# Kernel tuning notes

Measured on AMD Instinct MI355X. Metric: run time of the kernel, lower is better.

The kernel has to match this reference:

```python
import jax, jax.numpy as jnp
import numpy as np

N, D, H, C, OUT = 50000, 128, 2, 128, 2   # nodes, in-feat, heads, per-head width, classes
E = 800000
HC = H * C
NEG_SLOPE = 0.2


def setup_inputs() -> dict:
    key = jax.random.key(0)
    ks = jax.random.split(key, 12)
    x = jax.random.normal(ks[0], (N, D), dtype=jnp.float32)
    edge_index = jax.random.randint(ks[1], (2, E), 0, N, dtype=jnp.int64)
    def w(k, fan_in, shape):
        return jax.random.normal(k, shape, dtype=jnp.float32) / np.sqrt(fan_in)
    return {
        "x": x,
        "edge_index": edge_index,
        # layer 0: in D -> H*C
        "W0": w(ks[2], D, (D, HC)),
        "att_src0": w(ks[3], C, (H, C)),
        "att_dst0": w(ks[4], C, (H, C)),
        "b0": jnp.zeros((HC,), dtype=jnp.float32),
        # layer 1: in H*C -> H*C
        "W1": w(ks[5], HC, (HC, HC)),
        "att_src1": w(ks[6], C, (H, C)),
        "att_dst1": w(ks[7], C, (H, C)),
        "b1": jnp.zeros((HC,), dtype=jnp.float32),
        # final linear: H*C -> OUT (concat GAT output)
        "Wl": w(ks[8], HC, (HC, OUT)),
        "bl": jnp.zeros((OUT,), dtype=jnp.float32),
    }


def _gat_layer(x, src, dst, W, att_src, att_dst, b):
    """PyG GATConv (concat=True, negative_slope=0.2, self-loops already in src/dst)."""
    n = x.shape[0]
    h = (x @ W).reshape(n, H, C)                       # [N,H,C]
    a_s = jnp.einsum("nhc,hc->nh", h, att_src)         # [N,H]
    a_d = jnp.einsum("nhc,hc->nh", h, att_dst)         # [N,H]
    logits = jax.nn.leaky_relu(a_s[src] + a_d[dst], NEG_SLOPE)  # [E',H]
    m = jax.ops.segment_max(logits, dst, num_segments=n)
    e = jnp.exp(logits - m[dst])
    denom = jax.ops.segment_sum(e, dst, num_segments=n)
    alpha = e / (denom[dst] + 1e-16)                   # softmax over incoming edges
    msg = h[src] * alpha[:, :, None]                   # [E',H,C]
    out = jax.ops.segment_sum(msg, dst, num_segments=n)
    return out.reshape(n, HC) + b


def reference(x, edge_index, W0, att_src0, att_dst0, b0,
              W1, att_src1, att_dst1, b1, Wl, bl):
    n = x.shape[0]
    loop = jnp.arange(n, dtype=edge_index.dtype)
    src = jnp.concatenate([edge_index[0], loop])       # add self loops (GATConv default)
    dst = jnp.concatenate([edge_index[1], loop])
    h = _gat_layer(x, src, dst, W0, att_src0, att_dst0, b0)
    h = jnp.tanh(h)                                    # tanh between layers only
    h = _gat_layer(h, src, dst, W1, att_src1, att_dst1, b1)
    out = h @ Wl + bl
    return jax.nn.softmax(out, axis=1)
```

## Files before the change

kernel.cpp:

```cpp
#include <hip/hip_runtime.h>
#include <math.h>

constexpr int N_NODES = 50000;
constexpr int N_EDGES = 800000;
constexpr int TOT_E   = N_EDGES + N_NODES;
constexpr int HCv     = 256;
constexpr int MAXD    = 256;

constexpr int GY        = (N_NODES + 127) / 128;
constexpr int GPX       = (GY + 7) / 8;
constexpr int GEMM_BLKS = 8 * GPX * 4;

constexpr int PADSH = 5;

constexpr int PREP_CVT   = (N_NODES * 128 / 4 + 255) / 256;
constexpr int PREP_WT0   = 128;
constexpr int PREP_WT1   = 256;
constexpr int PREP_DEG   = (TOT_E + 255) / 256;
constexpr int PREP_ZERO  = (N_NODES * 12 / 4 + 255) / 256;
constexpr int PREP_C     = 1;
constexpr int PREP_BLKS  = PREP_CVT + PREP_WT0 + PREP_WT1 + PREP_DEG + PREP_ZERO + PREP_C;

typedef __attribute__((ext_vector_type(8))) short bf16x8;
typedef __attribute__((ext_vector_type(4))) float f32x4;
typedef __attribute__((ext_vector_type(2))) float f32x2;

__device__ __forceinline__ unsigned short f2bf(float f) {
    unsigned int u = __float_as_uint(f);
    unsigned int r = (u + 0x7fffu + ((u >> 16) & 1u)) >> 16;
    return (unsigned short)r;
}
__device__ __forceinline__ unsigned int f2bf_pack(float lo, float hi) {
    return (unsigned int)f2bf(lo) | ((unsigned int)f2bf(hi) << 16);
}
__device__ __forceinline__ float bf2f_lo(unsigned int packed) {
    return __uint_as_float(packed << 16);
}
__device__ __forceinline__ float bf2f_hi(unsigned int packed) {
    return __uint_as_float(packed & 0xffff0000u);
}

__device__ __forceinline__ void fma_row8_pk(const uint4 h, f32x2 al, f32x2* a2) {
    f32x2 p;
    p.x = bf2f_lo(h.x); p.y = bf2f_hi(h.x);
    a2[0] = __builtin_elementwise_fma(p, al, a2[0]);
    p.x = bf2f_lo(h.y); p.y = bf2f_hi(h.y);
    a2[1] = __builtin_elementwise_fma(p, al, a2[1]);
    p.x = bf2f_lo(h.z); p.y = bf2f_hi(h.z);
    a2[2] = __builtin_elementwise_fma(p, al, a2[2]);
    p.x = bf2f_lo(h.w); p.y = bf2f_hi(h.w);
    a2[3] = __builtin_elementwise_fma(p, al, a2[3]);
}


__global__ void zero_degp_k(uint4* __restrict__ degp4, int* __restrict__ total,
                            float* __restrict__ c2) {
    int i = blockIdx.x * blockDim.x + threadIdx.x;
    if (i < N_NODES * 32 / 4) degp4[i] = make_uint4(0, 0, 0, 0);
    if (blockIdx.x == 0 && threadIdx.x == 0) {
        *total = 0;
        c2[0] = 0.f;
        c2[1] = 0.f;
    }
}


__global__ __launch_bounds__(256) void prep_k(const float* __restrict__ x,
                                              unsigned short* __restrict__ xb,
                                              const float* __restrict__ W0,
                                              unsigned short* __restrict__ WT0,
                                              const float* __restrict__ W1,
                                              unsigned short* __restrict__ WT1,
                                              const int* __restrict__ ei,
                                              int* __restrict__ degp,
                                              float* __restrict__ a_sd,
                                              const float* __restrict__ Wl,
                                              const float* __restrict__ b1,
                                              const float* __restrict__ bl,
                                              float* __restrict__ c2) {
    int b = blockIdx.x;
    if (b < PREP_CVT) {
        int i = b * 256 + threadIdx.x;
        if (i < N_NODES * 128 / 4) {
            float4 v = *reinterpret_cast<const float4*>(x + (size_t)i * 4);
            ushort4 o;
            o.x = f2bf(v.x); o.y = f2bf(v.y); o.z = f2bf(v.z); o.w = f2bf(v.w);
            *reinterpret_cast<ushort4*>(xb + (size_t)i * 4) = o;
        }
        return;
    }
    b -= PREP_CVT;
    if (b < PREP_WT0) {
        int idx = b * 256 + threadIdx.x;
        int k = idx >> 8, n = idx & 255;
        WT0[(size_t)n * 128 + k] = f2bf(W0[idx]);
        return;
    }
    b -= PREP_WT0;
    if (b < PREP_WT1) {
        int idx = b * 256 + threadIdx.x;
        int k = idx >> 8, n = idx & 255;
        WT1[(size_t)n * 256 + k] = f2bf(W1[idx]);
        return;
    }
    b -= PREP_WT1;
    if (b < PREP_DEG) {
        int e = b * 256 + threadIdx.x;
        if (e < TOT_E) {
            int dst = (e < N_EDGES) ? ei[N_EDGES + e] : (e - N_EDGES);
            atomicAdd(&degp[dst << PADSH], 1);
        }
        return;
    }
    b -= PREP_DEG;
    if (b < PREP_ZERO) {
        int i = b * 256 + threadIdx.x;
        if (i < N_NODES * 3)
            *reinterpret_cast<float4*>(a_sd + (size_t)i * 4) = make_float4(0, 0, 0, 0);
        return;
    }
    {
        int k = threadIdx.x;
        int lane = k & 63;
        float bv = b1[k];
        float p0 = bv * Wl[k * 2 + 0];
        float p1 = bv * Wl[k * 2 + 1];
        if (k == 0) { p0 += bl[0]; p1 += bl[1]; }
#pragma unroll
        for (int off = 32; off; off >>= 1) {
            p0 += __shfl_xor(p0, off);
            p1 += __shfl_xor(p1, off);
        }
        if (lane == 0) {
            atomicAdd(&c2[0], p0);
            atomicAdd(&c2[1], p1);
        }
    }
}


__global__ void offsets_k(const int* __restrict__ degp, int* __restrict__ start,
                          int* __restrict__ deg, int* __restrict__ cursorp,
                          int* __restrict__ total) {
    int lane = threadIdx.x & 63;
    int node = blockIdx.x * blockDim.x + threadIdx.x;
    int d = (node < N_NODES) ? degp[node << PADSH] : 0;
    int pre = d;
#pragma unroll
    for (int off = 1; off < 64; off <<= 1) {
        int v = __shfl_up(pre, off);
        if (lane >= off) pre += v;
    }
    int wtot = __shfl(pre, 63);
    int base = 0;
    if (lane == 63) base = atomicAdd(total, wtot);
    base = __shfl(base, 63);
    int my = base + pre - d;
    if (node < N_NODES) {
        start[node] = my;
        deg[node] = d;
        cursorp[node << PADSH] = my;
    }
}

__global__ void scatter_k(const int* __restrict__ ei, int* __restrict__ cursorp,
                          int* __restrict__ colv) {
    int e = blockIdx.x * blockDim.x + threadIdx.x;
    if (e >= TOT_E) return;
    int srcv, dstv;
    if (e < N_EDGES) { srcv = ei[e]; dstv = ei[N_EDGES + e]; }
    else             { srcv = dstv = e - N_EDGES; }
    int pos = atomicAdd(&cursorp[dstv << PADSH], 1);
    colv[pos] = srcv;
}


template <int K, bool LAST>
__global__ __launch_bounds__(256) void mfma_gemm_att_k(
        const unsigned short* __restrict__ A,
        const unsigned short* __restrict__ BT,
        unsigned short* __restrict__ h16,
        const float* __restrict__ att_src, const float* __restrict__ att_dst,
        float* __restrict__ a_s, float* __restrict__ a_d, int M,
        const float* __restrict__ Wl, float* __restrict__ g) {
    const int bid = blockIdx.x;
    const int xcd = bid & 7;
    const int t   = bid >> 3;
    const int kx  = t & 3;
    const int gy  = xcd + 8 * (t >> 2);
    if (gy >= GY) return;

    const int lane = threadIdx.x & 63;
    const int wv = threadIdx.x >> 6;
    const int lm = lane & 15;
    const int g8 = (lane >> 4) * 8;
    const int row0 = gy * 128 + wv * 32;
    const int n0 = kx * 64;

    int ra0 = row0 + lm;       if (ra0 >= M) ra0 = M - 1;
    int ra1 = row0 + 16 + lm;  if (ra1 >= M) ra1 = M - 1;
    const unsigned short* pa0 = A + (size_t)ra0 * K + g8;
    const unsigned short* pa1 = A + (size_t)ra1 * K + g8;
    const unsigned short* pb  = BT + (size_t)(n0 + lm) * K + g8;

    f32x4 acc[2][4] = {};
#pragma unroll
    for (int kt = 0; kt < K; kt += 32) {
        bf16x8 a0 = *reinterpret_cast<const bf16x8*>(pa0 + kt);
        bf16x8 a1 = *reinterpret_cast<const bf16x8*>(pa1 + kt);
        bf16x8 b0 = *reinterpret_cast<const bf16x8*>(pb + kt);
        bf16x8 b1 = *reinterpret_cast<const bf16x8*>(pb + 16 * K + kt);
        bf16x8 b2 = *reinterpret_cast<const bf16x8*>(pb + 32 * K + kt);
        bf16x8 b3 = *reinterpret_cast<const bf16x8*>(pb + 48 * K + kt);
        acc[0][0] = __builtin_amdgcn_mfma_f32_16x16x32_bf16(a0, b0, acc[0][0], 0, 0, 0);
        acc[0][1] = __builtin_amdgcn_mfma_f32_16x16x32_bf16(a0, b1, acc[0][1], 0, 0, 0);
        acc[0][2] = __builtin_amdgcn_mfma_f32_16x16x32_bf16(a0, b2, acc[0][2], 0, 0, 0);
        acc[0][3] = __builtin_amdgcn_mfma_f32_16x16x32_bf16(a0, b3, acc[0][3], 0, 0, 0);
        acc[1][0] = __builtin_amdgcn_mfma_f32_16x16x32_bf16(a1, b0, acc[1][0], 0, 0, 0);
        acc[1][1] = __builtin_amdgcn_mfma_f32_16x16x32_bf16(a1, b1, acc[1][1], 0, 0, 0);
        acc[1][2] = __builtin_amdgcn_mfma_f32_16x16x32_bf16(a1, b2, acc[1][2], 0, 0, 0);
        acc[1][3] = __builtin_amdgcn_mfma_f32_16x16x32_bf16(a1, b3, acc[1][3], 0, 0, 0);
    }

    float as_c[4], ad_c[4], wl0_c[4], wl1_c[4];
#pragma unroll
    for (int j = 0; j < 4; ++j) {
        int c = n0 + j * 16 + lm;
        as_c[j] = att_src[c];
        ad_c[j] = att_dst[c];
        if (LAST) {
            wl0_c[j] = Wl[c * 2 + 0];
            wl1_c[j] = Wl[c * 2 + 1];
        }
    }
    const int head = n0 >> 7;

#pragma unroll
    for (int i = 0; i < 2; ++i) {
        float ps[4] = {}, pd[4] = {}, pg0[4] = {}, pg1[4] = {};
#pragma unroll
        for (int j = 0; j < 4; ++j)
#pragma unroll
            for (int r = 0; r < 4; ++r) {
                ps[r] += acc[i][j][r] * as_c[j];
                pd[r] += acc[i][j][r] * ad_c[j];
                if (LAST) {
                    pg0[r] += acc[i][j][r] * wl0_c[j];
                    pg1[r] += acc[i][j][r] * wl1_c[j];
                }
            }
#pragma unroll
        for (int off = 1; off < 16; off <<= 1)
#pragma unroll
            for (int r = 0; r < 4; ++r) {
                ps[r] += __shfl_xor(ps[r], off);
                pd[r] += __shfl_xor(pd[r], off);
                if (LAST) {
                    pg0[r] += __shfl_xor(pg0[r], off);
                    pg1[r] += __shfl_xor(pg1[r], off);
                }
            }
        if (lm == 0) {
            int rb = row0 + i * 16 + (lane >> 4) * 4;
#pragma unroll
            for (int r = 0; r < 4; ++r) {
                if (rb + r < M) {
                    atomicAdd(&a_s[(rb + r) * 2 + head], ps[r]);
                    atomicAdd(&a_d[(rb + r) * 2 + head], pd[r]);
                    if (LAST) {
                        atomicAdd(&g[(rb + r) * 4 + head * 2 + 0], pg0[r]);
                        atomicAdd(&g[(rb + r) * 4 + head * 2 + 1], pg1[r]);
                    }
                }
            }
        }
        if (!LAST) {
#pragma unroll
            for (int j = 0; j < 4; ++j)
#pragma unroll
                for (int r = 0; r < 4; ++r) {
                    int row = row0 + i * 16 + (lane >> 4) * 4 + r;
                    if (row < M)
                        h16[(size_t)row * HCv + n0 + j * 16 + lm] = f2bf(acc[i][j][r]);
                }
        }
    }
}


__device__ __forceinline__ float lrelu(float x) { return x > 0.f ? x : 0.2f * x; }

__global__ __launch_bounds__(256) void agg_k(const unsigned short* __restrict__ h16,
                      const float* __restrict__ a_s, const float* __restrict__ a_d,
                      const int* __restrict__ start, const int* __restrict__ deg,
                      const int* __restrict__ colv, const float* __restrict__ bias,
                      unsigned short* __restrict__ out16) {
    __shared__ float lexp[4][MAXD][2];
    const int lane = threadIdx.x & 63;
    const int wslot = threadIdx.x >> 6;
    const int node = blockIdx.x * 4 + wslot;
    if (node >= N_NODES) return;
    const int beg = start[node];
    const int degv = deg[node];
    const float ad0 = a_d[node * 2], ad1 = a_d[node * 2 + 1];
    const int* __restrict__ col = colv + beg;

    if (degv <= MAXD) {
        float s0 = 0.f, s1 = 0.f;
        for (int j = lane; j < degv; j += 64) {
            int s = col[j];
            float2 av = *reinterpret_cast<const float2*>(a_s + s * 2);
            float e0 = __expf(lrelu(av.x + ad0));
            float e1 = __expf(lrelu(av.y + ad1));
            *reinterpret_cast<float2*>(&lexp[wslot][j][0]) = make_float2(e0, e1);
            s0 += e0;
            s1 += e1;
        }
#pragma unroll
        for (int off = 32; off; off >>= 1) {
            s0 += __shfl_xor(s0, off);
            s1 += __shfl_xor(s1, off);
        }
        const float inv0 = 1.f / (s0 + 1e-16f);
        const float inv1 = 1.f / (s1 + 1e-16f);

        const int q = lane >> 4;
        const int lq = lane & 15;
        const int cb = lq * 16;
        const int head = lq >> 3;
        const float invh = head ? inv1 : inv0;
        const unsigned short* __restrict__ hp = h16 + cb;
        f32x2 acc2[8] = {};
        const int full = degv >> 2;
        for (int i = 0; i < full; ++i) {
            const int j = 4 * i + q;
            const int s = col[j];
            const float alpha = lexp[wslot][j][head] * invh;
            const f32x2 al = {alpha, alpha};
            const uint4* p = reinterpret_cast<const uint4*>(hp + (size_t)s * HCv);
            const uint4 h0 = p[0];
            const uint4 h1 = p[1];
            fma_row8_pk(h0, al, acc2);
            fma_row8_pk(h1, al, acc2 + 4);
        }
        {
            const int j = full * 4 + q;
            if (j < degv) {
                const int s = col[j];
                const float alpha = lexp[wslot][j][head] * invh;
                const f32x2 al = {alpha, alpha};
                const uint4* p = reinterpret_cast<const uint4*>(hp + (size_t)s * HCv);
                const uint4 h0 = p[0];
                const uint4 h1 = p[1];
                fma_row8_pk(h0, al, acc2);
                fma_row8_pk(h1, al, acc2 + 4);
            }
        }
        float acc[16];
#pragma unroll
        for (int c = 0; c < 8; ++c) {
            acc[2 * c]     = acc2[c].x;
            acc[2 * c + 1] = acc2[c].y;
        }
#pragma unroll
        for (int c = 0; c < 16; ++c) {
            acc[c] += __shfl_xor(acc[c], 16);
            acc[c] += __shfl_xor(acc[c], 32);
        }
        if (lane < 16) {
#pragma unroll
            for (int c = 0; c < 16; ++c) acc[c] = tanhf(acc[c] + bias[cb + c]);
            uint4 v0, v1;
            v0.x = f2bf_pack(acc[0], acc[1]);
            v0.y = f2bf_pack(acc[2], acc[3]);
            v0.z = f2bf_pack(acc[4], acc[5]);
            v0.w = f2bf_pack(acc[6], acc[7]);
            v1.x = f2bf_pack(acc[8], acc[9]);
            v1.y = f2bf_pack(acc[10], acc[11]);
            v1.z = f2bf_pack(acc[12], acc[13]);
            v1.w = f2bf_pack(acc[14], acc[15]);
            uint4* o = reinterpret_cast<uint4*>(out16 + (size_t)node * HCv + cb);
            o[0] = v0;
            o[1] = v1;
        }
    } else {
        const int end = beg + degv;
        float m0 = -INFINITY, m1 = -INFINITY;
        for (int e = beg + lane; e < end; e += 64) {
            int s = colv[e];
            m0 = fmaxf(m0, lrelu(a_s[s * 2] + ad0));
            m1 = fmaxf(m1, lrelu(a_s[s * 2 + 1] + ad1));
        }
#pragma unroll
        for (int off = 32; off; off >>= 1) {
            m0 = fmaxf(m0, __shfl_xor(m0, off));
            m1 = fmaxf(m1, __shfl_xor(m1, off));
        }
        float s0 = 0.f, s1 = 0.f;
        for (int e = beg + lane; e < end; e += 64) {
            int s = colv[e];
            s0 += __expf(lrelu(a_s[s * 2] + ad0) - m0);
            s1 += __expf(lrelu(a_s[s * 2 + 1] + ad1) - m1);
        }
#pragma unroll
        for (int off = 32; off; off >>= 1) {
            s0 += __shfl_xor(s0, off);
            s1 += __shfl_xor(s1, off);
        }
        float inv0 = 1.f / (s0 + 1e-16f);
        float inv1 = 1.f / (s1 + 1e-16f);
        const int head = lane >> 5;
        const float mh  = head ? m1 : m0;
        const float ih  = head ? inv1 : inv0;
        const float adh = head ? ad1 : ad0;
        const int cbase = lane * 4;
        float acc0 = 0.f, acc1 = 0.f, acc2 = 0.f, acc3 = 0.f;
        for (int e = beg; e < end; ++e) {
            int s = colv[e];
            float l = lrelu(a_s[s * 2 + head] + adh);
            float alpha = __expf(l - mh) * ih;
            uint2 hv = *reinterpret_cast<const uint2*>(h16 + (size_t)s * HCv + cbase);
            acc0 = fmaf(bf2f_lo(hv.x), alpha, acc0);
            acc1 = fmaf(bf2f_hi(hv.x), alpha, acc1);
            acc2 = fmaf(bf2f_lo(hv.y), alpha, acc2);
            acc3 = fmaf(bf2f_hi(hv.y), alpha, acc3);
        }
        float o0 = tanhf(acc0 + bias[cbase + 0]);
        float o1 = tanhf(acc1 + bias[cbase + 1]);
        float o2 = tanhf(acc2 + bias[cbase + 2]);
        float o3 = tanhf(acc3 + bias[cbase + 3]);
        ushort4 v;
        v.x = f2bf(o0); v.y = f2bf(o1); v.z = f2bf(o2); v.w = f2bf(o3);
        *reinterpret_cast<ushort4*>(out16 + (size_t)node * HCv + cbase) = v;
    }
}


__global__ __launch_bounds__(256) void agg_final_k(
        const float* __restrict__ a_s, const float* __restrict__ a_d,
        const float* __restrict__ g, const int* __restrict__ start,
        const int* __restrict__ deg, const int* __restrict__ colv,
        const float* __restrict__ c2, float* __restrict__ out) {
    const int lane = threadIdx.x & 63;
    const int node = blockIdx.x * 4 + (threadIdx.x >> 6);
    if (node >= N_NODES) return;
    const int beg = start[node];
    const int degv = deg[node];
    const float ad0 = a_d[node * 2], ad1 = a_d[node * 2 + 1];
    const int* __restrict__ col = colv + beg;

    float s0 = 0.f, s1 = 0.f, A00 = 0.f, A01 = 0.f, A10 = 0.f, A11 = 0.f;
    for (int j = lane; j < degv; j += 64) {
        int s = col[j];
        float2 av = *reinterpret_cast<const float2*>(a_s + s * 2);
        float4 gv = *reinterpret_cast<const float4*>(g + s * 4);
        float e0 = __expf(lrelu(av.x + ad0));
        float e1 = __expf(lrelu(av.y + ad1));
        s0 += e0;
        s1 += e1;
        A00 = fmaf(e0, gv.x, A00);
        A01 = fmaf(e0, gv.y, A01);
        A10 = fmaf(e1, gv.z, A10);
        A11 = fmaf(e1, gv.w, A11);
    }
#pragma unroll
    for (int off = 32; off; off >>= 1) {
        s0  += __shfl_xor(s0, off);
        s1  += __shfl_xor(s1, off);
        A00 += __shfl_xor(A00, off);
        A01 += __shfl_xor(A01, off);
        A10 += __shfl_xor(A10, off);
        A11 += __shfl_xor(A11, off);
    }
    if (lane == 0) {
        float i0 = 1.f / (s0 + 1e-16f), i1 = 1.f / (s1 + 1e-16f);
        float z0 = A00 * i0 + A10 * i1 + c2[0];
        float z1 = A01 * i0 + A11 * i1 + c2[1];
        float mx = fmaxf(z0, z1);
        float e0 = __expf(z0 - mx), e1 = __expf(z1 - mx);
        float inv = 1.f / (e0 + e1);
        out[node * 2 + 0] = e0 * inv;
        out[node * 2 + 1] = e1 * inv;
    }
}


extern "C" void kernel_launch(void* const* d_in, const int* in_sizes, int n_in,
                              void* d_out, int out_size, void* d_ws, size_t ws_size,
                              hipStream_t stream) {
    const float* x        = (const float*)d_in[0];
    const int*   ei       = (const int*)d_in[1];
    const float* W0       = (const float*)d_in[2];
    const float* att_src0 = (const float*)d_in[3];
    const float* att_dst0 = (const float*)d_in[4];
    const float* b0       = (const float*)d_in[5];
    const float* W1       = (const float*)d_in[6];
    const float* att_src1 = (const float*)d_in[7];
    const float* att_dst1 = (const float*)d_in[8];
    const float* b1       = (const float*)d_in[9];
    const float* Wl       = (const float*)d_in[10];
    const float* bl       = (const float*)d_in[11];
    float* out = (float*)d_out;

    unsigned short* xb     = (unsigned short*)d_ws;
    unsigned short* h16    = xb + (size_t)N_NODES * 128;
    unsigned short* hact16 = h16 + (size_t)N_NODES * HCv;
    unsigned short* WT0    = hact16 + (size_t)N_NODES * HCv;
    unsigned short* WT1    = WT0 + 256 * 128;
    int*   degp  = (int*)(WT1 + 256 * 256);
    float* a_sd  = (float*)(degp + (size_t)N_NODES * 32);
    float* as0   = a_sd;
    float* ad0   = as0 + N_NODES * 2;
    float* as1   = ad0 + N_NODES * 2;
    float* ad1   = as1 + N_NODES * 2;
    float* gbuf  = ad1 + N_NODES * 2;
    int* cursorp = (int*)(gbuf + (size_t)N_NODES * 4);
    int* deg     = cursorp + (size_t)N_NODES * 32;
    int* start   = deg + N_NODES;
    int* total   = start + N_NODES;
    float* c2    = (float*)(total + 1);
    int* colv    = (int*)(c2 + 2);

    zero_degp_k<<<(N_NODES * 32 / 4 + 255) / 256, 256, 0, stream>>>((uint4*)degp,
                                                                    total, c2);
    prep_k<<<PREP_BLKS, 256, 0, stream>>>(x, xb, W0, WT0, W1, WT1, ei, degp, a_sd,
                                          Wl, b1, bl, c2);

    offsets_k<<<(N_NODES + 255) / 256, 256, 0, stream>>>(degp, start, deg, cursorp, total);
    scatter_k<<<(TOT_E + 255) / 256, 256, 0, stream>>>(ei, cursorp, colv);

    int nn4 = (N_NODES + 3) / 4;

    mfma_gemm_att_k<128, false><<<GEMM_BLKS, 256, 0, stream>>>(
        xb, WT0, h16, att_src0, att_dst0, as0, ad0, N_NODES, nullptr, nullptr);
    agg_k<<<nn4, 256, 0, stream>>>(h16, as0, ad0, start, deg, colv, b0, hact16);

    mfma_gemm_att_k<256, true><<<GEMM_BLKS, 256, 0, stream>>>(
        hact16, WT1, nullptr, att_src1, att_dst1, as1, ad1, N_NODES, Wl, gbuf);
    agg_final_k<<<nn4, 256, 0, stream>>>(as1, ad1, gbuf, start, deg, colv, c2, out);
}
```

Before: 315.9 us.

## Aggregate raw features before the layer-0 GEMM and fold W1 into per-node projections

```diff
diff --git a/kernel.cpp b/kernel.cpp
--- a/kernel.cpp
+++ b/kernel.cpp
@@ -13,13 +13,13 @@
 
 constexpr int PADSH = 5;
 
-constexpr int PREP_CVT   = (N_NODES * 128 / 4 + 255) / 256;
-constexpr int PREP_WT0   = 128;
-constexpr int PREP_WT1   = 256;
-constexpr int PREP_DEG   = (TOT_E + 255) / 256;
-constexpr int PREP_ZERO  = (N_NODES * 12 / 4 + 255) / 256;
-constexpr int PREP_C     = 1;
-constexpr int PREP_BLKS  = PREP_CVT + PREP_WT0 + PREP_WT1 + PREP_DEG + PREP_ZERO + PREP_C;
+constexpr int PREP_CVT  = (N_NODES * 128 / 4 + 255) / 256;
+constexpr int PREP_WT0  = 128;
+constexpr int PREP_DEG  = (TOT_E + 255) / 256;
+constexpr int PREP_ZA   = (N_NODES * 8 / 4 + 255) / 256;
+constexpr int PREP_SKIN = (N_NODES + 15) / 16;
+constexpr int PREP_C    = 1;
+constexpr int PREP_BLKS = PREP_CVT + PREP_WT0 + PREP_DEG + PREP_ZA + PREP_SKIN + PREP_C;
 
 typedef __attribute__((ext_vector_type(8))) short bf16x8;
 typedef __attribute__((ext_vector_type(4))) float f32x4;
@@ -40,44 +40,68 @@
     return __uint_as_float(packed & 0xffff0000u);
 }
 
-__device__ __forceinline__ void fma_row8_pk(const uint4 h, f32x2 al, f32x2* a2) {
-    f32x2 p;
-    p.x = bf2f_lo(h.x); p.y = bf2f_hi(h.x);
-    a2[0] = __builtin_elementwise_fma(p, al, a2[0]);
-    p.x = bf2f_lo(h.y); p.y = bf2f_hi(h.y);
-    a2[1] = __builtin_elementwise_fma(p, al, a2[1]);
-    p.x = bf2f_lo(h.z); p.y = bf2f_hi(h.z);
-    a2[2] = __builtin_elementwise_fma(p, al, a2[2]);
-    p.x = bf2f_lo(h.w); p.y = bf2f_hi(h.w);
-    a2[3] = __builtin_elementwise_fma(p, al, a2[3]);
-}
-
-
-__global__ void zero_degp_k(uint4* __restrict__ degp4, int* __restrict__ total,
-                            float* __restrict__ c2) {
+__device__ __forceinline__ float lrelu(float x) { return x > 0.f ? x : 0.2f * x; }
+
+
+__global__ __launch_bounds__(256) void zero_pre_k(uint4* __restrict__ degp4,
+        int* __restrict__ total, float* __restrict__ c2,
+        const float* __restrict__ W0, const float* __restrict__ att_src0,
+        const float* __restrict__ att_dst0,
+        const float* __restrict__ W1, const float* __restrict__ att_src1,
+        const float* __restrict__ att_dst1, const float* __restrict__ Wl,
+        float* __restrict__ w0buf, float* __restrict__ pv) {
     int i = blockIdx.x * blockDim.x + threadIdx.x;
     if (i < N_NODES * 32 / 4) degp4[i] = make_uint4(0, 0, 0, 0);
-    if (blockIdx.x == 0 && threadIdx.x == 0) {
-        *total = 0;
-        c2[0] = 0.f;
-        c2[1] = 0.f;
+    if (blockIdx.x == 0) {
+        if (threadIdx.x == 0) { *total = 0; c2[0] = 0.f; c2[1] = 0.f; }
+        int k = threadIdx.x;
+        float v0 = 0, v1 = 0, v2 = 0, v3 = 0, v4 = 0, v5 = 0, v6 = 0, v7 = 0;
+        const float* wr = W1 + (size_t)k * 256;
+        for (int c = 0; c < 128; ++c) {
+            float wv = wr[c];
+            v0 = fmaf(wv, att_src1[c], v0);
+            v2 = fmaf(wv, att_dst1[c], v2);
+            v4 = fmaf(wv, Wl[c * 2 + 0], v4);
+            v5 = fmaf(wv, Wl[c * 2 + 1], v5);
+        }
+        for (int c = 128; c < 256; ++c) {
+            float wv = wr[c];
+            v1 = fmaf(wv, att_src1[c], v1);
+            v3 = fmaf(wv, att_dst1[c], v3);
+            v6 = fmaf(wv, Wl[c * 2 + 0], v6);
+            v7 = fmaf(wv, Wl[c * 2 + 1], v7);
+        }
+        float* p = pv + (size_t)k * 8;
+        p[0] = v0; p[1] = v1; p[2] = v2; p[3] = v3;
+        p[4] = v4; p[5] = v5; p[6] = v6; p[7] = v7;
+        if (k < 128) {
+            float w0v = 0, w1v = 0, w2v = 0, w3v = 0;
+            const float* wr0 = W0 + (size_t)k * 256;
+            for (int c = 0; c < 128; ++c) {
+                float wv = wr0[c];
+                w0v = fmaf(wv, att_src0[c], w0v);
+                w2v = fmaf(wv, att_dst0[c], w2v);
+            }
+            for (int c = 128; c < 256; ++c) {
+                float wv = wr0[c];
+                w1v = fmaf(wv, att_src0[c], w1v);
+                w3v = fmaf(wv, att_dst0[c], w3v);
+            }
+            float* q = w0buf + (size_t)k * 4;
+            q[0] = w0v; q[1] = w1v; q[2] = w2v; q[3] = w3v;
+        }
     }
 }
 
 
 __global__ __launch_bounds__(256) void prep_k(const float* __restrict__ x,
-                                              unsigned short* __restrict__ xb,
-                                              const float* __restrict__ W0,
-                                              unsigned short* __restrict__ WT0,
-                                              const float* __restrict__ W1,
-                                              unsigned short* __restrict__ WT1,
-                                              const int* __restrict__ ei,
-                                              int* __restrict__ degp,
-                                              float* __restrict__ a_sd,
-                                              const float* __restrict__ Wl,
-                                              const float* __restrict__ b1,
-                                              const float* __restrict__ bl,
-                                              float* __restrict__ c2) {
+        unsigned short* __restrict__ xb, const float* __restrict__ W0,
+        unsigned short* __restrict__ WT0, const int* __restrict__ ei,
+        int* __restrict__ degp, float* __restrict__ asd1,
+        const float* __restrict__ w0buf, float* __restrict__ a_s,
+        float* __restrict__ a_d, const float* __restrict__ Wl,
+        const float* __restrict__ b1, const float* __restrict__ bl,
+        float* __restrict__ c2) {
     int b = blockIdx.x;
     if (b < PREP_CVT) {
         int i = b * 256 + threadIdx.x;
@@ -97,13 +121,6 @@
         return;
     }
     b -= PREP_WT0;
-    if (b < PREP_WT1) {
-        int idx = b * 256 + threadIdx.x;
-        int k = idx >> 8, n = idx & 255;
-        WT1[(size_t)n * 256 + k] = f2bf(W1[idx]);
-        return;
-    }
-    b -= PREP_WT1;
     if (b < PREP_DEG) {
         int e = b * 256 + threadIdx.x;
         if (e < TOT_E) {
@@ -113,10 +130,43 @@
         return;
     }
     b -= PREP_DEG;
-    if (b < PREP_ZERO) {
+    if (b < PREP_ZA) {
         int i = b * 256 + threadIdx.x;
-        if (i < N_NODES * 3)
-            *reinterpret_cast<float4*>(a_sd + (size_t)i * 4) = make_float4(0, 0, 0, 0);
+        if (i < N_NODES * 2)
+            *reinterpret_cast<float4*>(asd1 + (size_t)i * 4) = make_float4(0, 0, 0, 0);
+        return;
+    }
+    b -= PREP_ZA;
+    if (b < PREP_SKIN) {
+        int lane = threadIdx.x & 63;
+        int sub = lane >> 4;
+        int lq = lane & 15;
+        int node = b * 16 + (threadIdx.x >> 6) * 4 + sub;
+        if (node < N_NODES) {
+            const float* xr = x + (size_t)node * 128 + lq * 8;
+            const float4* wv = reinterpret_cast<const float4*>(w0buf) + lq * 8;
+            float s0 = 0, s1 = 0, d0 = 0, d1 = 0;
+#pragma unroll
+            for (int t = 0; t < 8; ++t) {
+                float xv = xr[t];
+                float4 w = wv[t];
+                s0 = fmaf(xv, w.x, s0);
+                s1 = fmaf(xv, w.y, s1);
+                d0 = fmaf(xv, w.z, d0);
+                d1 = fmaf(xv, w.w, d1);
+            }
+#pragma unroll
+            for (int off = 1; off < 16; off <<= 1) {
+                s0 += __shfl_xor(s0, off);
+                s1 += __shfl_xor(s1, off);
+                d0 += __shfl_xor(d0, off);
+                d1 += __shfl_xor(d1, off);
+            }
+            if (lq == 0) {
+                *reinterpret_cast<float2*>(a_s + node * 2) = make_float2(s0, s1);
+                *reinterpret_cast<float2*>(a_d + node * 2) = make_float2(d0, d1);
+            }
+        }
         return;
     }
     {
@@ -175,126 +225,11 @@
 }
 
 
-template <int K, bool LAST>
-__global__ __launch_bounds__(256) void mfma_gemm_att_k(
-        const unsigned short* __restrict__ A,
-        const unsigned short* __restrict__ BT,
-        unsigned short* __restrict__ h16,
-        const float* __restrict__ att_src, const float* __restrict__ att_dst,
-        float* __restrict__ a_s, float* __restrict__ a_d, int M,
-        const float* __restrict__ Wl, float* __restrict__ g) {
-    const int bid = blockIdx.x;
-    const int xcd = bid & 7;
-    const int t   = bid >> 3;
-    const int kx  = t & 3;
-    const int gy  = xcd + 8 * (t >> 2);
-    if (gy >= GY) return;
-
-    const int lane = threadIdx.x & 63;
-    const int wv = threadIdx.x >> 6;
-    const int lm = lane & 15;
-    const int g8 = (lane >> 4) * 8;
-    const int row0 = gy * 128 + wv * 32;
-    const int n0 = kx * 64;
-
-    int ra0 = row0 + lm;       if (ra0 >= M) ra0 = M - 1;
-    int ra1 = row0 + 16 + lm;  if (ra1 >= M) ra1 = M - 1;
-    const unsigned short* pa0 = A + (size_t)ra0 * K + g8;
-    const unsigned short* pa1 = A + (size_t)ra1 * K + g8;
-    const unsigned short* pb  = BT + (size_t)(n0 + lm) * K + g8;
-
-    f32x4 acc[2][4] = {};
-#pragma unroll
-    for (int kt = 0; kt < K; kt += 32) {
-        bf16x8 a0 = *reinterpret_cast<const bf16x8*>(pa0 + kt);
-        bf16x8 a1 = *reinterpret_cast<const bf16x8*>(pa1 + kt);
-        bf16x8 b0 = *reinterpret_cast<const bf16x8*>(pb + kt);
-        bf16x8 b1 = *reinterpret_cast<const bf16x8*>(pb + 16 * K + kt);
-        bf16x8 b2 = *reinterpret_cast<const bf16x8*>(pb + 32 * K + kt);
-        bf16x8 b3 = *reinterpret_cast<const bf16x8*>(pb + 48 * K + kt);
-        acc[0][0] = __builtin_amdgcn_mfma_f32_16x16x32_bf16(a0, b0, acc[0][0], 0, 0, 0);
-        acc[0][1] = __builtin_amdgcn_mfma_f32_16x16x32_bf16(a0, b1, acc[0][1], 0, 0, 0);
-        acc[0][2] = __builtin_amdgcn_mfma_f32_16x16x32_bf16(a0, b2, acc[0][2], 0, 0, 0);
-        acc[0][3] = __builtin_amdgcn_mfma_f32_16x16x32_bf16(a0, b3, acc[0][3], 0, 0, 0);
-        acc[1][0] = __builtin_amdgcn_mfma_f32_16x16x32_bf16(a1, b0, acc[1][0], 0, 0, 0);
-        acc[1][1] = __builtin_amdgcn_mfma_f32_16x16x32_bf16(a1, b1, acc[1][1], 0, 0, 0);
-        acc[1][2] = __builtin_amdgcn_mfma_f32_16x16x32_bf16(a1, b2, acc[1][2], 0, 0, 0);
-        acc[1][3] = __builtin_amdgcn_mfma_f32_16x16x32_bf16(a1, b3, acc[1][3], 0, 0, 0);
-    }
-
-    float as_c[4], ad_c[4], wl0_c[4], wl1_c[4];
-#pragma unroll
-    for (int j = 0; j < 4; ++j) {
-        int c = n0 + j * 16 + lm;
-        as_c[j] = att_src[c];
-        ad_c[j] = att_dst[c];
-        if (LAST) {
-            wl0_c[j] = Wl[c * 2 + 0];
-            wl1_c[j] = Wl[c * 2 + 1];
-        }
-    }
-    const int head = n0 >> 7;
-
-#pragma unroll
-    for (int i = 0; i < 2; ++i) {
-        float ps[4] = {}, pd[4] = {}, pg0[4] = {}, pg1[4] = {};
-#pragma unroll
-        for (int j = 0; j < 4; ++j)
-#pragma unroll
-            for (int r = 0; r < 4; ++r) {
-                ps[r] += acc[i][j][r] * as_c[j];
-                pd[r] += acc[i][j][r] * ad_c[j];
-                if (LAST) {
-                    pg0[r] += acc[i][j][r] * wl0_c[j];
-                    pg1[r] += acc[i][j][r] * wl1_c[j];
-                }
-            }
-#pragma unroll
-        for (int off = 1; off < 16; off <<= 1)
-#pragma unroll
-            for (int r = 0; r < 4; ++r) {
-                ps[r] += __shfl_xor(ps[r], off);
-                pd[r] += __shfl_xor(pd[r], off);
-                if (LAST) {
-                    pg0[r] += __shfl_xor(pg0[r], off);
-                    pg1[r] += __shfl_xor(pg1[r], off);
-                }
-            }
-        if (lm == 0) {
-            int rb = row0 + i * 16 + (lane >> 4) * 4;
-#pragma unroll
-            for (int r = 0; r < 4; ++r) {
-                if (rb + r < M) {
-                    atomicAdd(&a_s[(rb + r) * 2 + head], ps[r]);
-                    atomicAdd(&a_d[(rb + r) * 2 + head], pd[r]);
-                    if (LAST) {
-                        atomicAdd(&g[(rb + r) * 4 + head * 2 + 0], pg0[r]);
-                        atomicAdd(&g[(rb + r) * 4 + head * 2 + 1], pg1[r]);
-                    }
-                }
-            }
-        }
-        if (!LAST) {
-#pragma unroll
-            for (int j = 0; j < 4; ++j)
-#pragma unroll
-                for (int r = 0; r < 4; ++r) {
-                    int row = row0 + i * 16 + (lane >> 4) * 4 + r;
-                    if (row < M)
-                        h16[(size_t)row * HCv + n0 + j * 16 + lm] = f2bf(acc[i][j][r]);
-                }
-        }
-    }
-}
-
-
-__device__ __forceinline__ float lrelu(float x) { return x > 0.f ? x : 0.2f * x; }
-
-__global__ __launch_bounds__(256) void agg_k(const unsigned short* __restrict__ h16,
+__global__ __launch_bounds__(256) void agg0x_k(const unsigned short* __restrict__ xb,
                       const float* __restrict__ a_s, const float* __restrict__ a_d,
                       const int* __restrict__ start, const int* __restrict__ deg,
-                      const int* __restrict__ colv, const float* __restrict__ bias,
-                      unsigned short* __restrict__ out16) {
+                      const int* __restrict__ colv,
+                      unsigned short* __restrict__ xagg) {
     __shared__ float lexp[4][MAXD][2];
     const int lane = threadIdx.x & 63;
     const int wslot = threadIdx.x >> 6;
@@ -326,41 +261,61 @@
 
         const int q = lane >> 4;
         const int lq = lane & 15;
-        const int cb = lq * 16;
-        const int head = lq >> 3;
-        const float invh = head ? inv1 : inv0;
-        const unsigned short* __restrict__ hp = h16 + cb;
-        f32x2 acc2[8] = {};
+        const unsigned short* __restrict__ xp = xb + lq * 8;
+        f32x2 aA[4] = {};
+        f32x2 aB[4] = {};
         const int full = degv >> 2;
         for (int i = 0; i < full; ++i) {
             const int j = 4 * i + q;
             const int s = col[j];
-            const float alpha = lexp[wslot][j][head] * invh;
-            const f32x2 al = {alpha, alpha};
-            const uint4* p = reinterpret_cast<const uint4*>(hp + (size_t)s * HCv);
-            const uint4 h0 = p[0];
-            const uint4 h1 = p[1];
-            fma_row8_pk(h0, al, acc2);
-            fma_row8_pk(h1, al, acc2 + 4);
+            float2 ee = *reinterpret_cast<float2*>(&lexp[wslot][j][0]);
+            const uint4 hv = *reinterpret_cast<const uint4*>(xp + (size_t)s * 128);
+            const f32x2 al0 = {ee.x, ee.x};
+            const f32x2 al1 = {ee.y, ee.y};
+            f32x2 p;
+            p.x = bf2f_lo(hv.x); p.y = bf2f_hi(hv.x);
+            aA[0] = __builtin_elementwise_fma(p, al0, aA[0]);
+            aB[0] = __builtin_elementwise_fma(p, al1, aB[0]);
+            p.x = bf2f_lo(hv.y); p.y = bf2f_hi(hv.y);
+            aA[1] = __builtin_elementwise_fma(p, al0, aA[1]);
+            aB[1] = __builtin_elementwise_fma(p, al1, aB[1]);
+            p.x = bf2f_lo(hv.z); p.y = bf2f_hi(hv.z);
+            aA[2] = __builtin_elementwise_fma(p, al0, aA[2]);
+            aB[2] = __builtin_elementwise_fma(p, al1, aB[2]);
+            p.x = bf2f_lo(hv.w); p.y = bf2f_hi(hv.w);
+            aA[3] = __builtin_elementwise_fma(p, al0, aA[3]);
+            aB[3] = __builtin_elementwise_fma(p, al1, aB[3]);
         }
         {
             const int j = full * 4 + q;
             if (j < degv) {
                 const int s = col[j];
-                const float alpha = lexp[wslot][j][head] * invh;
-                const f32x2 al = {alpha, alpha};
-                const uint4* p = reinterpret_cast<const uint4*>(hp + (size_t)s * HCv);
-                const uint4 h0 = p[0];
-                const uint4 h1 = p[1];
-                fma_row8_pk(h0, al, acc2);
-                fma_row8_pk(h1, al, acc2 + 4);
+                float2 ee = *reinterpret_cast<float2*>(&lexp[wslot][j][0]);
+                const uint4 hv = *reinterpret_cast<const uint4*>(xp + (size_t)s * 128);
+                const f32x2 al0 = {ee.x, ee.x};
+                const f32x2 al1 = {ee.y, ee.y};
+                f32x2 p;
+                p.x = bf2f_lo(hv.x); p.y = bf2f_hi(hv.x);
+                aA[0] = __builtin_elementwise_fma(p, al0, aA[0]);
+                aB[0] = __builtin_elementwise_fma(p, al1, aB[0]);
+                p.x = bf2f_lo(hv.y); p.y = bf2f_hi(hv.y);
+                aA[1] = __builtin_elementwise_fma(p, al0, aA[1]);
+                aB[1] = __builtin_elementwise_fma(p, al1, aB[1]);
+                p.x = bf2f_lo(hv.z); p.y = bf2f_hi(hv.z);
+                aA[2] = __builtin_elementwise_fma(p, al0, aA[2]);
+                aB[2] = __builtin_elementwise_fma(p, al1, aB[2]);
+                p.x = bf2f_lo(hv.w); p.y = bf2f_hi(hv.w);
+                aA[3] = __builtin_elementwise_fma(p, al0, aA[3]);
+                aB[3] = __builtin_elementwise_fma(p, al1, aB[3]);
             }
         }
         float acc[16];
 #pragma unroll
-        for (int c = 0; c < 8; ++c) {
-            acc[2 * c]     = acc2[c].x;
-            acc[2 * c + 1] = acc2[c].y;
+        for (int c = 0; c < 4; ++c) {
+            acc[2 * c]     = aA[c].x;
+            acc[2 * c + 1] = aA[c].y;
+            acc[8 + 2 * c]     = aB[c].x;
+            acc[8 + 2 * c + 1] = aB[c].y;
         }
 #pragma unroll
         for (int c = 0; c < 16; ++c) {
@@ -369,7 +324,9 @@
         }
         if (lane < 16) {
 #pragma unroll
-            for (int c = 0; c < 16; ++c) acc[c] = tanhf(acc[c] + bias[cb + c]);
+            for (int c = 0; c < 8; ++c)  acc[c] *= inv0;
+#pragma unroll
+            for (int c = 8; c < 16; ++c) acc[c] *= inv1;
             uint4 v0, v1;
             v0.x = f2bf_pack(acc[0], acc[1]);
             v0.y = f2bf_pack(acc[2], acc[3]);
@@ -379,9 +336,8 @@
             v1.y = f2bf_pack(acc[10], acc[11]);
             v1.z = f2bf_pack(acc[12], acc[13]);
             v1.w = f2bf_pack(acc[14], acc[15]);
-            uint4* o = reinterpret_cast<uint4*>(out16 + (size_t)node * HCv + cb);
-            o[0] = v0;
-            o[1] = v1;
+            *reinterpret_cast<uint4*>(xagg + (size_t)node * 256 + lq * 8) = v0;
+            *reinterpret_cast<uint4*>(xagg + (size_t)node * 256 + 128 + lq * 8) = v1;
         }
     } else {
         const int end = beg + degv;
@@ -409,36 +365,130 @@
         }
         float inv0 = 1.f / (s0 + 1e-16f);
         float inv1 = 1.f / (s1 + 1e-16f);
-        const int head = lane >> 5;
-        const float mh  = head ? m1 : m0;
-        const float ih  = head ? inv1 : inv0;
-        const float adh = head ? ad1 : ad0;
-        const int cbase = lane * 4;
-        float acc0 = 0.f, acc1 = 0.f, acc2 = 0.f, acc3 = 0.f;
+        const int cbase = lane * 2;
+        float a00 = 0.f, a01 = 0.f, a10 = 0.f, a11 = 0.f;
         for (int e = beg; e < end; ++e) {
             int s = colv[e];
-            float l = lrelu(a_s[s * 2 + head] + adh);
-            float alpha = __expf(l - mh) * ih;
-            uint2 hv = *reinterpret_cast<const uint2*>(h16 + (size_t)s * HCv + cbase);
-            acc0 = fmaf(bf2f_lo(hv.x), alpha, acc0);
-            acc1 = fmaf(bf2f_hi(hv.x), alpha, acc1);
-            acc2 = fmaf(bf2f_lo(hv.y), alpha, acc2);
-            acc3 = fmaf(bf2f_hi(hv.y), alpha, acc3);
-        }
-        float o0 = tanhf(acc0 + bias[cbase + 0]);
-        float o1 = tanhf(acc1 + bias[cbase + 1]);
-        float o2 = tanhf(acc2 + bias[cbase + 2]);
-        float o3 = tanhf(acc3 + bias[cbase + 3]);
-        ushort4 v;
-        v.x = f2bf(o0); v.y = f2bf(o1); v.z = f2bf(o2); v.w = f2bf(o3);
-        *reinterpret_cast<ushort4*>(out16 + (size_t)node * HCv + cbase) = v;
+            float2 av = *reinterpret_cast<const float2*>(a_s + s * 2);
+            float al0 = __expf(lrelu(av.x + ad0) - m0) * inv0;
+            float al1 = __expf(lrelu(av.y + ad1) - m1) * inv1;
+            unsigned int xv = *reinterpret_cast<const unsigned int*>(
+                xb + (size_t)s * 128 + cbase);
+            float x0 = bf2f_lo(xv), x1 = bf2f_hi(xv);
+            a00 = fmaf(x0, al0, a00);
+            a01 = fmaf(x1, al0, a01);
+            a10 = fmaf(x0, al1, a10);
+            a11 = fmaf(x1, al1, a11);
+        }
+        *reinterpret_cast<unsigned int*>(xagg + (size_t)node * 256 + cbase) =
+            f2bf_pack(a00, a01);
+        *reinterpret_cast<unsigned int*>(xagg + (size_t)node * 256 + 128 + cbase) =
+            f2bf_pack(a10, a11);
+    }
+}
+
+
+__global__ __launch_bounds__(256) void gemm_tanh_k(
+        const unsigned short* __restrict__ A,
+        const unsigned short* __restrict__ BT,
+        const float* __restrict__ b0,
+        const float* __restrict__ pv,
+        float* __restrict__ asd1, int M) {
+    const int bid = blockIdx.x;
+    const int xcd = bid & 7;
+    const int t   = bid >> 3;
+    const int kx  = t & 3;
+    const int gy  = xcd + 8 * (t >> 2);
+    if (gy >= GY) return;
+
+    const int lane = threadIdx.x & 63;
+    const int wv = threadIdx.x >> 6;
+    const int lm = lane & 15;
+    const int g8 = (lane >> 4) * 8;
+    const int row0 = gy * 128 + wv * 32;
+    const int n0 = kx * 64;
+    const int head = n0 >> 7;
+
+    int ra0 = row0 + lm;       if (ra0 >= M) ra0 = M - 1;
+    int ra1 = row0 + 16 + lm;  if (ra1 >= M) ra1 = M - 1;
+    const unsigned short* pa0 = A + (size_t)ra0 * 256 + head * 128 + g8;
+    const unsigned short* pa1 = A + (size_t)ra1 * 256 + head * 128 + g8;
+    const unsigned short* pb  = BT + (size_t)(n0 + lm) * 128 + g8;
+
+    f32x4 acc[2][4] = {};
+#pragma unroll
+    for (int kt = 0; kt < 128; kt += 32) {
+        bf16x8 a0 = *reinterpret_cast<const bf16x8*>(pa0 + kt);
+        bf16x8 a1 = *reinterpret_cast<const bf16x8*>(pa1 + kt);
+        bf16x8 b0f = *reinterpret_cast<const bf16x8*>(pb + kt);
+        bf16x8 b1f = *reinterpret_cast<const bf16x8*>(pb + 16 * 128 + kt);
+        bf16x8 b2f = *reinterpret_cast<const bf16x8*>(pb + 32 * 128 + kt);
+        bf16x8 b3f = *reinterpret_cast<const bf16x8*>(pb + 48 * 128 + kt);
+        acc[0][0] = __builtin_amdgcn_mfma_f32_16x16x32_bf16(a0, b0f, acc[0][0], 0, 0, 0);
+        acc[0][1] = __builtin_amdgcn_mfma_f32_16x16x32_bf16(a0, b1f, acc[0][1], 0, 0, 0);
+        acc[0][2] = __builtin_amdgcn_mfma_f32_16x16x32_bf16(a0, b2f, acc[0][2], 0, 0, 0);
+        acc[0][3] = __builtin_amdgcn_mfma_f32_16x16x32_bf16(a0, b3f, acc[0][3], 0, 0, 0);
+        acc[1][0] = __builtin_amdgcn_mfma_f32_16x16x32_bf16(a1, b0f, acc[1][0], 0, 0, 0);
+        acc[1][1] = __builtin_amdgcn_mfma_f32_16x16x32_bf16(a1, b1f, acc[1][1], 0, 0, 0);
+        acc[1][2] = __builtin_amdgcn_mfma_f32_16x16x32_bf16(a1, b2f, acc[1][2], 0, 0, 0);
+        acc[1][3] = __builtin_amdgcn_mfma_f32_16x16x32_bf16(a1, b3f, acc[1][3], 0, 0, 0);
+    }
+
+    float bc[4];
+    float4 pA[4], pB[4];
+#pragma unroll
+    for (int j = 0; j < 4; ++j) {
+        int c = n0 + j * 16 + lm;
+        bc[j] = b0[c];
+        pA[j] = *reinterpret_cast<const float4*>(pv + (size_t)c * 8);
+        pB[j] = *reinterpret_cast<const float4*>(pv + (size_t)c * 8 + 4);
+    }
+
+#pragma unroll
+    for (int i = 0; i < 2; ++i) {
+        float pr[8][4];
+#pragma unroll
+        for (int p = 0; p < 8; ++p)
+#pragma unroll
+            for (int r = 0; r < 4; ++r) pr[p][r] = 0.f;
+#pragma unroll
+        for (int j = 0; j < 4; ++j)
+#pragma unroll
+            for (int r = 0; r < 4; ++r) {
+                float th = tanhf(acc[i][j][r] + bc[j]);
+                pr[0][r] = fmaf(th, pA[j].x, pr[0][r]);
+                pr[1][r] = fmaf(th, pA[j].y, pr[1][r]);
+                pr[2][r] = fmaf(th, pA[j].z, pr[2][r]);
+                pr[3][r] = fmaf(th, pA[j].w, pr[3][r]);
+                pr[4][r] = fmaf(th, pB[j].x, pr[4][r]);
+                pr[5][r] = fmaf(th, pB[j].y, pr[5][r]);
+                pr[6][r] = fmaf(th, pB[j].z, pr[6][r]);
+                pr[7][r] = fmaf(th, pB[j].w, pr[7][r]);
+            }
+#pragma unroll
+        for (int off = 1; off < 16; off <<= 1)
+#pragma unroll
+            for (int p = 0; p < 8; ++p)
+#pragma unroll
+                for (int r = 0; r < 4; ++r)
+                    pr[p][r] += __shfl_xor(pr[p][r], off);
+        if (lm == 0) {
+            int rb = row0 + i * 16 + (lane >> 4) * 4;
+#pragma unroll
+            for (int r = 0; r < 4; ++r) {
+                if (rb + r < M) {
+                    float* dst = asd1 + (size_t)(rb + r) * 8;
+#pragma unroll
+                    for (int p = 0; p < 8; ++p) atomicAdd(&dst[p], pr[p][r]);
+                }
+            }
+        }
     }
 }
 
 
 __global__ __launch_bounds__(256) void agg_final_k(
-        const float* __restrict__ a_s, const float* __restrict__ a_d,
-        const float* __restrict__ g, const int* __restrict__ start,
+        const float* __restrict__ asd1, const int* __restrict__ start,
         const int* __restrict__ deg, const int* __restrict__ colv,
         const float* __restrict__ c2, float* __restrict__ out) {
     const int lane = threadIdx.x & 63;
@@ -446,16 +496,18 @@
     if (node >= N_NODES) return;
     const int beg = start[node];
     const int degv = deg[node];
-    const float ad0 = a_d[node * 2], ad1 = a_d[node * 2 + 1];
+    const float ad0 = asd1[node * 8 + 2];
+    const float ad1v = asd1[node * 8 + 3];
     const int* __restrict__ col = colv + beg;
 
     float s0 = 0.f, s1 = 0.f, A00 = 0.f, A01 = 0.f, A10 = 0.f, A11 = 0.f;
     for (int j = lane; j < degv; j += 64) {
         int s = col[j];
-        float2 av = *reinterpret_cast<const float2*>(a_s + s * 2);
-        float4 gv = *reinterpret_cast<const float4*>(g + s * 4);
+        const float* rs = asd1 + (size_t)s * 8;
+        float2 av = *reinterpret_cast<const float2*>(rs);
+        float4 gv = *reinterpret_cast<const float4*>(rs + 4);
         float e0 = __expf(lrelu(av.x + ad0));
-        float e1 = __expf(lrelu(av.y + ad1));
+        float e1 = __expf(lrelu(av.y + ad1v));
         s0 += e0;
         s1 += e1;
         A00 = fmaf(e0, gv.x, A00);
@@ -502,40 +554,36 @@
     const float* bl       = (const float*)d_in[11];
     float* out = (float*)d_out;
 
-    unsigned short* xb     = (unsigned short*)d_ws;
-    unsigned short* h16    = xb + (size_t)N_NODES * 128;
-    unsigned short* hact16 = h16 + (size_t)N_NODES * HCv;
-    unsigned short* WT0    = hact16 + (size_t)N_NODES * HCv;
-    unsigned short* WT1    = WT0 + 256 * 128;
-    int*   degp  = (int*)(WT1 + 256 * 256);
-    float* a_sd  = (float*)(degp + (size_t)N_NODES * 32);
-    float* as0   = a_sd;
+    unsigned short* xb   = (unsigned short*)d_ws;
+    unsigned short* xagg = xb + (size_t)N_NODES * 128;
+    unsigned short* WT0  = xagg + (size_t)N_NODES * 256;
+    float* w0buf = (float*)(WT0 + 256 * 128);
+    float* pv    = w0buf + 128 * 4;
+    float* as0   = pv + 256 * 8;
     float* ad0   = as0 + N_NODES * 2;
-    float* as1   = ad0 + N_NODES * 2;
-    float* ad1   = as1 + N_NODES * 2;
-    float* gbuf  = ad1 + N_NODES * 2;
-    int* cursorp = (int*)(gbuf + (size_t)N_NODES * 4);
+    float* asd1  = ad0 + N_NODES * 2;
+    int*   degp  = (int*)(asd1 + (size_t)N_NODES * 8);
+    int* cursorp = degp + (size_t)N_NODES * 32;
     int* deg     = cursorp + (size_t)N_NODES * 32;
     int* start   = deg + N_NODES;
     int* total   = start + N_NODES;
     float* c2    = (float*)(total + 1);
     int* colv    = (int*)(c2 + 2);
 
-    zero_degp_k<<<(N_NODES * 32 / 4 + 255) / 256, 256, 0, stream>>>((uint4*)degp,
-                                                                    total, c2);
-    prep_k<<<PREP_BLKS, 256, 0, stream>>>(x, xb, W0, WT0, W1, WT1, ei, degp, a_sd,
-                                          Wl, b1, bl, c2);
+    zero_pre_k<<<(N_NODES * 32 / 4 + 255) / 256, 256, 0, stream>>>(
+        (uint4*)degp, total, c2, W0, att_src0, att_dst0,
+        W1, att_src1, att_dst1, Wl, w0buf, pv);
+
+    prep_k<<<PREP_BLKS, 256, 0, stream>>>(x, xb, W0, WT0, ei, degp, asd1,
+                                          w0buf, as0, ad0, Wl, b1, bl, c2);
 
     offsets_k<<<(N_NODES + 255) / 256, 256, 0, stream>>>(degp, start, deg, cursorp, total);
     scatter_k<<<(TOT_E + 255) / 256, 256, 0, stream>>>(ei, cursorp, colv);
 
     int nn4 = (N_NODES + 3) / 4;
 
-    mfma_gemm_att_k<128, false><<<GEMM_BLKS, 256, 0, stream>>>(
-        xb, WT0, h16, att_src0, att_dst0, as0, ad0, N_NODES, nullptr, nullptr);
-    agg_k<<<nn4, 256, 0, stream>>>(h16, as0, ad0, start, deg, colv, b0, hact16);
-
-    mfma_gemm_att_k<256, true><<<GEMM_BLKS, 256, 0, stream>>>(
-        hact16, WT1, nullptr, att_src1, att_dst1, as1, ad1, N_NODES, Wl, gbuf);
-    agg_final_k<<<nn4, 256, 0, stream>>>(as1, ad1, gbuf, start, deg, colv, c2, out);
-}
+    agg0x_k<<<nn4, 256, 0, stream>>>(xb, as0, ad0, start, deg, colv, xagg);
+    gemm_tanh_k<<<GEMM_BLKS, 256, 0, stream>>>(xagg, WT0, b0, pv, asd1, N_NODES);
+
+    agg_final_k<<<nn4, 256, 0, stream>>>(asd1, start, deg, colv, c2, out);
+}
```

Result: slower. 330.1 us (+4.5%).
